# Kernel tuning notes

Measured on AMD Instinct MI355X. Metric: run time of the kernel, lower is better.

The kernel has to match this reference:

```python
import jax, jax.numpy as jnp
import numpy as np

B, R, L, D = 32, 48, 128, 64
PRIOR_HOURS = 48.0


def setup_inputs() -> dict:
    key = jax.random.key(0)
    ks = jax.random.split(key, 9)
    X = jax.random.normal(ks[0], (B, L, D), dtype=jnp.float32)
    # observation times in [0, prior_hours]
    T = jax.random.uniform(ks[1], (B, L, D), dtype=jnp.float32) * PRIOR_HOURS
    # observation mask (0/1 float, as used in the paper)
    M = (jax.random.uniform(ks[2], (B, L, D)) > 0.5).astype(jnp.float32)
    PD = jax.random.normal(ks[3], (B, L, D), dtype=jnp.float32)
    # learned parameters (glorot-uniform-like small init)
    alpha = jax.random.normal(ks[4], (R, 1, 1), dtype=jnp.float32) * 0.1
    w_v = jax.random.normal(ks[5], (R, L, D), dtype=jnp.float32) * 0.05
    w_t = jax.random.normal(ks[6], (R, L, D, 4), dtype=jnp.float32) * 0.05
    b_t = jax.random.normal(ks[7], (R, L, D, 1), dtype=jnp.float32) * 0.05
    b_v = jax.random.normal(ks[8], (R, 1, D), dtype=jnp.float32) * 0.05
    # fixed reference time grid (buffer, not trained)
    ref_time = jnp.linspace(0.0, PRIOR_HOURS, R, dtype=jnp.float32).reshape(R, 1, 1)
    return {"X": X, "T": T, "M": M, "PD": PD, "alpha": alpha,
            "w_v": w_v, "w_t": w_t, "b_t": b_t, "b_v": b_v, "ref_time": ref_time}


def reference(X, T, M, PD, alpha, w_v, w_t, b_t, b_v, ref_time):
    # broadcast over R ref time points instead of tf.tile: [B,R,L,D]
    dist = jnp.abs(T[:, None, :, :] - ref_time)          # type_distance == 'abs'
    kernel = jnp.exp(-jax.nn.relu(alpha) * dist)          # [B,R,L,D]
    intensity = jax.nn.relu(X[:, None, :, :] * kernel)    # [B,R,L,D]
    shp = dist.shape
    feats = jnp.stack([
        jnp.broadcast_to(X[:, None, :, :], shp),
        intensity,
        jnp.broadcast_to(M[:, None, :, :], shp),
        jnp.broadcast_to(PD[:, None, :, :], shp),
    ], axis=-1)                                            # [B,R,L,D,4] == tf.concat on axis 4
    # reduce_sum(w_t * feats + b_t, axis=4): broadcast b_t over the 4-axis -> 4*b_t
    latent = jax.nn.relu(jnp.einsum('rlde,brlde->brld', w_t, feats) + 4.0 * b_t[..., 0])
    # reduce_sum(w_v * latent + b_v, axis=2): b_v broadcast over L -> L*b_v
    out = jax.nn.relu(jnp.einsum('rld,brld->brd', w_v, latent) + L * b_v[:, 0, :])
    return out  # [B, R, D]
```

## Files before the change

### kernel.cpp

```cpp
#include <hip/hip_runtime.h>

#define B 32
#define R 48
#define L 128
#define D 64

template<int TR_, int TB_, int NS_>
__global__ __launch_bounds__(256) void alnn_part1_t(
    const float* __restrict__ X, const float* __restrict__ T,
    const float* __restrict__ M, const float* __restrict__ PD,
    const float* __restrict__ alpha, const float* __restrict__ w_v,
    const float* __restrict__ w_t, const float* __restrict__ b_t,
    const float* __restrict__ ref_time, float* __restrict__ ws)
{
    constexpr int NBT = B / TB_;
    constexpr int LCH = L / NS_;
    constexpr int LW  = LCH / 4;
    static_assert(LW >= 1, "need at least 1 l per wave");
    const int id   = blockIdx.x;
    const int s    = id % NS_;
    const int rest = id / NS_;
    const int bt   = rest % NBT;
    const int rt   = rest / NBT;
    const int d    = threadIdx.x & 63;
    const int ly   = threadIdx.x >> 6;
    const int r0 = rt * TR_, b0 = bt * TB_;

    float a_[TR_], rt_[TR_];
    #pragma unroll
    for (int r = 0; r < TR_; ++r) {
        a_[r]  = fmaxf(alpha[r0 + r], 0.0f);
        rt_[r] = ref_time[r0 + r];
    }

    float acc[TR_][TB_];
    #pragma unroll
    for (int r = 0; r < TR_; ++r)
        #pragma unroll
        for (int b = 0; b < TB_; ++b) acc[r][b] = 0.0f;

    const float4* __restrict__ w_t4 = reinterpret_cast<const float4*>(w_t);
    const int l0 = s * LCH + ly * LW;

    #pragma unroll
    for (int li = 0; li < LW; ++li) {
        const int l = l0 + li;
        float4 wt[TR_]; float btv[TR_], wv[TR_];
        #pragma unroll
        for (int r = 0; r < TR_; ++r) {
            const int iw = ((r0 + r) * L + l) * D + d;
            wt[r]  = w_t4[iw];
            btv[r] = 4.0f * b_t[iw];
            wv[r]  = w_v[iw];
        }
        float xv[TB_], tv[TB_], mv[TB_], pv[TB_];
        #pragma unroll
        for (int b = 0; b < TB_; ++b) {
            const int ix = ((b0 + b) * L + l) * D + d;
            xv[b] = X[ix];  tv[b] = T[ix];  mv[b] = M[ix];  pv[b] = PD[ix];
        }
        #pragma unroll
        for (int r = 0; r < TR_; ++r) {
            #pragma unroll
            for (int b = 0; b < TB_; ++b) {
                const float dist  = fabsf(tv[b] - rt_[r]);
                const float kern  = __expf(-a_[r] * dist);
                const float inten = fmaxf(xv[b] * kern, 0.0f);
                const float ssum  = fmaf(wt[r].x, xv[b],
                                    fmaf(wt[r].y, inten,
                                    fmaf(wt[r].z, mv[b],
                                    fmaf(wt[r].w, pv[b], btv[r]))));
                acc[r][b] = fmaf(wv[r], fmaxf(ssum, 0.0f), acc[r][b]);
            }
        }
    }

    __shared__ float red[4][TR_ * TB_][64];
    #pragma unroll
    for (int r = 0; r < TR_; ++r)
        #pragma unroll
        for (int b = 0; b < TB_; ++b)
            red[ly][r * TB_ + b][d] = acc[r][b];
    __syncthreads();

    #pragma unroll
    for (int p = ly; p < TR_ * TB_; p += 4) {
        const int r = p / TB_, b = p % TB_;
        const float v = red[0][p][d] + red[1][p][d] + red[2][p][d] + red[3][p][d];
        ws[(((size_t)s * B + (b0 + b)) * R + (r0 + r)) * D + d] = v;
    }
}

template<int NS_>
__global__ __launch_bounds__(256) void alnn_part2_t(
    const float* __restrict__ ws, const float* __restrict__ b_v,
    float* __restrict__ out)
{
    const int i = blockIdx.x * 256 + threadIdx.x;
    const int d = i & 63;
    const int r = (i >> 6) % R;
    const int b = i / (R * D);
    float sum = 0.0f;
    #pragma unroll
    for (int s = 0; s < NS_; ++s)
        sum += ws[(((size_t)s * B + b) * R + r) * D + d];
    out[i] = fmaxf(sum + (float)L * b_v[r * D + d], 0.0f);
}

__global__ __launch_bounds__(256) void alnn_fallback(
    const float* __restrict__ X, const float* __restrict__ T,
    const float* __restrict__ M, const float* __restrict__ PD,
    const float* __restrict__ alpha, const float* __restrict__ w_v,
    const float* __restrict__ w_t, const float* __restrict__ b_t,
    const float* __restrict__ b_v, const float* __restrict__ ref_time,
    float* __restrict__ out)
{
    const int br = blockIdx.x;
    const int b  = br / R;
    const int r  = br - b * R;
    const int d  = threadIdx.x & 63;
    const int ly = threadIdx.x >> 6;

    const float a  = fmaxf(alpha[r], 0.0f);
    const float rt = ref_time[r];
    const int baseX = b * L * D + d;
    const int baseW = r * L * D + d;

    float acc = 0.0f;
    const int l0 = ly * 32;
    #pragma unroll 4
    for (int li = 0; li < 32; ++li) {
        const int l  = l0 + li;
        const int ix = baseX + l * D;
        const int iw = baseW + l * D;
        const float x  = X[ix], t = T[ix], m = M[ix], pd = PD[ix];
        const float dist  = fabsf(t - rt);
        const float kern  = __expf(-a * dist);
        const float inten = fmaxf(x * kern, 0.0f);
        const float4 wt = reinterpret_cast<const float4*>(w_t)[iw];
        const float bt  = b_t[iw];
        float s = fmaf(wt.x, x, fmaf(wt.y, inten, fmaf(wt.z, m, fmaf(wt.w, pd, 4.0f * bt))));
        acc = fmaf(w_v[iw], fmaxf(s, 0.0f), acc);
    }
    __shared__ float red[4][64];
    red[ly][d] = acc;
    __syncthreads();
    if (ly == 0) {
        const float sum = red[0][d] + red[1][d] + red[2][d] + red[3][d];
        out[(b * R + r) * D + d] = fmaxf(sum + (float)L * b_v[r * D + d], 0.0f);
    }
}

extern "C" void kernel_launch(void* const* d_in, const int* in_sizes, int n_in,
                              void* d_out, int out_size, void* d_ws, size_t ws_size,
                              hipStream_t stream) {
    const float* X  = (const float*)d_in[0];
    const float* T  = (const float*)d_in[1];
    const float* M  = (const float*)d_in[2];
    const float* PD = (const float*)d_in[3];
    const float* alpha = (const float*)d_in[4];
    const float* w_v   = (const float*)d_in[5];
    const float* w_t   = (const float*)d_in[6];
    const float* b_t   = (const float*)d_in[7];
    const float* b_v   = (const float*)d_in[8];
    const float* ref_time = (const float*)d_in[9];
    float* out = (float*)d_out;
    float* ws  = (float*)d_ws;

    const size_t ws32 = (size_t)32 * B * R * D * sizeof(float);
    const size_t ws16 = (size_t)16 * B * R * D * sizeof(float);
    const size_t ws4  = (size_t) 4 * B * R * D * sizeof(float);

    if (ws_size >= ws32) {
        hipLaunchKernelGGL((alnn_part1_t<4, 8, 32>), dim3(1536), dim3(256), 0, stream,
                           X, T, M, PD, alpha, w_v, w_t, b_t, ref_time, ws);
        hipLaunchKernelGGL((alnn_part2_t<32>), dim3(B * R * D / 256), dim3(256), 0, stream,
                           ws, b_v, out);
    } else if (ws_size >= ws16) {
        hipLaunchKernelGGL((alnn_part1_t<4, 4, 16>), dim3(1536), dim3(256), 0, stream,
                           X, T, M, PD, alpha, w_v, w_t, b_t, ref_time, ws);
        hipLaunchKernelGGL((alnn_part2_t<16>), dim3(B * R * D / 256), dim3(256), 0, stream,
                           ws, b_v, out);
    } else if (ws_size >= ws4) {
        hipLaunchKernelGGL((alnn_part1_t<2, 2, 4>), dim3(1536), dim3(256), 0, stream,
                           X, T, M, PD, alpha, w_v, w_t, b_t, ref_time, ws);
        hipLaunchKernelGGL((alnn_part2_t<4>), dim3(B * R * D / 256), dim3(256), 0, stream,
                           ws, b_v, out);
    } else {
        hipLaunchKernelGGL(alnn_fallback, dim3(B * R), dim3(256), 0, stream,
                           X, T, M, PD, alpha, w_v, w_t, b_t, b_v, ref_time, out);
    }
}
```

Before: 19.50 us.

## Split batch across waves instead of L to drop LDS reduction in part1

```diff
diff --git a/kernel.cpp b/kernel.cpp
--- a/kernel.cpp
+++ b/kernel.cpp
@@ -4,6 +4,99 @@
 #define R 48
 #define L 128
 #define D 64
+
+template<int TR_, int TBW_, int LCH_>
+__global__ __launch_bounds__(256) void alnn_part1s(
+    const float* __restrict__ X, const float* __restrict__ T,
+    const float* __restrict__ M, const float* __restrict__ PD,
+    const float* __restrict__ alpha, const float* __restrict__ w_v,
+    const float* __restrict__ w_t, const float* __restrict__ b_t,
+    const float* __restrict__ ref_time, float* __restrict__ ws)
+{
+    constexpr int TBB = 4 * TBW_;
+    constexpr int NBT = B / TBB;
+    constexpr int NS  = L / LCH_;
+    const int id = blockIdx.x;
+    const int s  = id % NS;
+    const int bt = (id / NS) % NBT;
+    const int rt = id / (NS * NBT);
+    const int d  = threadIdx.x & 63;
+    const int ly = threadIdx.x >> 6;
+    const int r0 = rt * TR_;
+    const int b0 = bt * TBB + ly * TBW_;
+
+    float a_[TR_], rt_[TR_];
+    #pragma unroll
+    for (int r = 0; r < TR_; ++r) {
+        a_[r]  = fmaxf(alpha[r0 + r], 0.0f);
+        rt_[r] = ref_time[r0 + r];
+    }
+
+    float acc[TR_][TBW_];
+    #pragma unroll
+    for (int r = 0; r < TR_; ++r)
+        #pragma unroll
+        for (int b = 0; b < TBW_; ++b) acc[r][b] = 0.0f;
+
+    const float4* __restrict__ w_t4 = reinterpret_cast<const float4*>(w_t);
+    const int l0 = s * LCH_;
+
+    #pragma unroll
+    for (int li = 0; li < LCH_; ++li) {
+        const int l = l0 + li;
+        float4 wt[TR_]; float btv[TR_], wv[TR_];
+        #pragma unroll
+        for (int r = 0; r < TR_; ++r) {
+            const int iw = ((r0 + r) * L + l) * D + d;
+            wt[r]  = w_t4[iw];
+            btv[r] = 4.0f * b_t[iw];
+            wv[r]  = w_v[iw];
+        }
+        float xv[TBW_], xp[TBW_], tv[TBW_], mv[TBW_], pv[TBW_];
+        #pragma unroll
+        for (int b = 0; b < TBW_; ++b) {
+            const int ix = ((b0 + b) * L + l) * D + d;
+            xv[b] = X[ix];  tv[b] = T[ix];  mv[b] = M[ix];  pv[b] = PD[ix];
+            xp[b] = fmaxf(xv[b], 0.0f);
+        }
+        #pragma unroll
+        for (int r = 0; r < TR_; ++r) {
+            #pragma unroll
+            for (int b = 0; b < TBW_; ++b) {
+                const float dist  = fabsf(tv[b] - rt_[r]);
+                const float kern  = __expf(-a_[r] * dist);
+                const float inten = xp[b] * kern;
+                const float ssum  = fmaf(wt[r].x, xv[b],
+                                    fmaf(wt[r].y, inten,
+                                    fmaf(wt[r].z, mv[b],
+                                    fmaf(wt[r].w, pv[b], btv[r]))));
+                acc[r][b] = fmaf(wv[r], fmaxf(ssum, 0.0f), acc[r][b]);
+            }
+        }
+    }
+
+    #pragma unroll
+    for (int r = 0; r < TR_; ++r)
+        #pragma unroll
+        for (int b = 0; b < TBW_; ++b)
+            ws[(((size_t)s * B + (b0 + b)) * R + (r0 + r)) * D + d] = acc[r][b];
+}
+
+template<int NS_>
+__global__ __launch_bounds__(256) void alnn_part2_t(
+    const float* __restrict__ ws, const float* __restrict__ b_v,
+    float* __restrict__ out)
+{
+    const int i = blockIdx.x * 256 + threadIdx.x;
+    const int d = i & 63;
+    const int r = (i >> 6) % R;
+    const int b = i / (R * D);
+    float sum = 0.0f;
+    #pragma unroll
+    for (int s = 0; s < NS_; ++s)
+        sum += ws[(((size_t)s * B + b) * R + r) * D + d];
+    out[i] = fmaxf(sum + (float)L * b_v[r * D + d], 0.0f);
+}
 
 template<int TR_, int TB_, int NS_>
 __global__ __launch_bounds__(256) void alnn_part1_t(
@@ -16,7 +109,6 @@
     constexpr int NBT = B / TB_;
     constexpr int LCH = L / NS_;
     constexpr int LW  = LCH / 4;
-    static_assert(LW >= 1, "need at least 1 l per wave");
     const int id   = blockIdx.x;
     const int s    = id % NS_;
     const int rest = id / NS_;
@@ -32,7 +124,6 @@
         a_[r]  = fmaxf(alpha[r0 + r], 0.0f);
         rt_[r] = ref_time[r0 + r];
     }
-
     float acc[TR_][TB_];
     #pragma unroll
     for (int r = 0; r < TR_; ++r)
@@ -82,29 +173,12 @@
         for (int b = 0; b < TB_; ++b)
             red[ly][r * TB_ + b][d] = acc[r][b];
     __syncthreads();
-
     #pragma unroll
     for (int p = ly; p < TR_ * TB_; p += 4) {
         const int r = p / TB_, b = p % TB_;
         const float v = red[0][p][d] + red[1][p][d] + red[2][p][d] + red[3][p][d];
         ws[(((size_t)s * B + (b0 + b)) * R + (r0 + r)) * D + d] = v;
     }
-}
-
-template<int NS_>
-__global__ __launch_bounds__(256) void alnn_part2_t(
-    const float* __restrict__ ws, const float* __restrict__ b_v,
-    float* __restrict__ out)
-{
-    const int i = blockIdx.x * 256 + threadIdx.x;
-    const int d = i & 63;
-    const int r = (i >> 6) % R;
-    const int b = i / (R * D);
-    float sum = 0.0f;
-    #pragma unroll
-    for (int s = 0; s < NS_; ++s)
-        sum += ws[(((size_t)s * B + b) * R + r) * D + d];
-    out[i] = fmaxf(sum + (float)L * b_v[r * D + d], 0.0f);
 }
 
 __global__ __launch_bounds__(256) void alnn_fallback(
@@ -172,7 +246,7 @@
     const size_t ws4  = (size_t) 4 * B * R * D * sizeof(float);
 
     if (ws_size >= ws32) {
-        hipLaunchKernelGGL((alnn_part1_t<4, 8, 32>), dim3(1536), dim3(256), 0, stream,
+        hipLaunchKernelGGL((alnn_part1s<4, 2, 4>), dim3(1536), dim3(256), 0, stream,
                            X, T, M, PD, alpha, w_v, w_t, b_t, ref_time, ws);
         hipLaunchKernelGGL((alnn_part2_t<32>), dim3(B * R * D / 256), dim3(256), 0, stream,
                            ws, b_v, out);
```

New measurement: 19.43 us. No clear change (-0.4%).
